# Kernel optimization log

Hardware: AMD Instinct MI355X
Metric: run time of the kernel (lower is better)

Reference implementation:

```python
import jax, jax.numpy as jnp
import numpy as np

HID = 512       # hidden_dim (embed/LSTM input)
HDE = 512       # hidden_dim_de == attn_channels (required by conv_att channel count)
NCLS = 7000
LSEQ = 40
B = 128
FH, FW = 8, 32


def setup_inputs() -> dict:
    key = jax.random.key(0)
    ks = jax.random.split(key, 16)
    s = 0.05
    inp = {
        "hidden_en": jax.random.normal(ks[0], (1, B, HID), jnp.float32),
        "x_em": jax.random.normal(ks[1], (B, HDE, FH, FW), jnp.float32),
        "att_x_em": jax.random.normal(ks[2], (B, FH * FW, HDE), jnp.float32),
        "target": jax.random.randint(ks[3], (B, LSEQ), 0, NCLS),
        "feature_h": FH,
        "feature_w": FW,
        # parameters
        "embed_w": jax.random.normal(ks[4], (NCLS, HID), jnp.float32) * s,
        "W_ih": jax.random.normal(ks[5], (4 * HDE, HID), jnp.float32) * s,   # LSTMCell input weights (i,f,g,o)
        "W_hh": jax.random.normal(ks[6], (4 * HDE, HDE), jnp.float32) * s,
        "b_ih": jax.random.normal(ks[7], (4 * HDE,), jnp.float32) * s,
        "b_hh": jax.random.normal(ks[8], (4 * HDE,), jnp.float32) * s,
        "hem_w": jax.random.normal(ks[9], (HDE, HDE), jnp.float32) * s,     # 1x1 conv h_em as matrix
        "hem_b": jax.random.normal(ks[10], (HDE,), jnp.float32) * s,
        "attw_w": jax.random.normal(ks[11], (HDE,), jnp.float32) * s,       # 1x1 conv conv_att -> 1 channel
        "attw_b": jax.random.normal(ks[12], (), jnp.float32) * s,
        "lin_w": jax.random.normal(ks[13], (NCLS, HDE + HDE), jnp.float32) * s,
        "lin_b": jax.random.normal(ks[14], (NCLS,), jnp.float32) * s,
    }
    return inp


def _decode(hidden_en, x_em, att_x_em, target, embed_w, W_ih, W_hh, b_ih, b_hh,
            hem_w, hem_b, attw_w, attw_b, lin_w, lin_b):
    L = target.shape[1]
    # teacher-forced inputs: step 0 uses hidden_en[-1], step t>=1 uses embed(target[:, t-1])
    xt0 = hidden_en[-1]                                   # [B, HID]
    xts = jnp.concatenate([xt0[None], jnp.transpose(embed_w[target[:, : L - 1]], (1, 0, 2))], axis=0)  # [L,B,HID]
    xg_all = jnp.einsum('lbi,gi->lbg', xts, W_ih) + b_ih  # precompute input gates [L,B,4H]
    Bn = x_em.shape[0]
    h0 = jnp.zeros((Bn, HDE), x_em.dtype)
    c0 = jnp.zeros((Bn, HDE), x_em.dtype)

    def step(carry, xg):
        h, c = carry
        gates = xg + h @ W_hh.T + b_hh
        i, f, g, o = jnp.split(gates, 4, axis=-1)
        c = jax.nn.sigmoid(f) * c + jax.nn.sigmoid(i) * jnp.tanh(g)
        h = jax.nn.sigmoid(o) * jnp.tanh(c)
        # additive attention (dropout treated as identity for determinism)
        hem = h @ hem_w.T + hem_b                          # [B, C]
        feat = jnp.tanh(x_em + hem[:, :, None, None])      # [B, C, H, W]
        feat_att = jnp.einsum('bchw,c->bhw', feat, attw_w) + attw_b
        alpha = jax.nn.softmax(feat_att.reshape(Bn, -1), axis=-1)  # [B, HW]
        att = jnp.einsum('bn,bnd->bd', alpha, att_x_em)    # [B, C]
        scores = jax.nn.log_softmax(jnp.concatenate([h, att], -1) @ lin_w.T + lin_b)
        return (h, c), scores

    _, ys = jax.lax.scan(step, (h0, c0), xg_all)           # ys: [L, B, NCLS]
    return jnp.transpose(ys, (1, 0, 2))                    # [B, L, NCLS]


def reference(hidden_en, x_em, att_x_em, target, feature_h, feature_w,
              embed_w, W_ih, W_hh, b_ih, b_hh, hem_w, hem_b, attw_w, attw_b,
              lin_w, lin_b):
    return _decode(hidden_en, x_em, att_x_em, target, embed_w, W_ih, W_hh,
                   b_ih, b_hh, hem_w, hem_b, attw_w, attw_b, lin_w, lin_b)
```

## Files before the change

### kernel.cpp

```cpp
#include <hip/hip_runtime.h>

#define B_    128
#define HIDD  512
#define NCLS  7000
#define NPAD  7040
#define LSEQ  40
#define MROWS 5120

typedef __attribute__((ext_vector_type(8))) short bf16x8;
typedef __attribute__((ext_vector_type(4))) float f32x4;

__device__ __forceinline__ unsigned short f2bf(float x) {
  union { float f; unsigned u; } v; v.f = x;
  unsigned r = v.u + 0x7fffu + ((v.u >> 16) & 1u);
  return (unsigned short)(r >> 16);
}
__device__ __forceinline__ float bf2f(unsigned short h) {
  union { unsigned u; float f; } v; v.u = ((unsigned)h) << 16;
  return v.f;
}
__device__ __forceinline__ float sigm(float x) { return 1.f / (1.f + __expf(-x)); }
__device__ __forceinline__ float tanh_f(float x) {
  float e = __expf(2.f * x);
  return 1.f - 2.f / (e + 1.f);
}

__global__ __launch_bounds__(256) void k_cvt(const float* __restrict__ src,
                                             unsigned short* __restrict__ dst, int n4) {
  int i = blockIdx.x * 256 + threadIdx.x;
  if (i >= n4) return;
  float4 v = ((const float4*)src)[i];
  ushort4 o; o.x = f2bf(v.x); o.y = f2bf(v.y); o.z = f2bf(v.z); o.w = f2bf(v.w);
  ((ushort4*)dst)[i] = o;
}

__global__ __launch_bounds__(256) void k_linpad(const float* __restrict__ lw,
                                                unsigned short* __restrict__ dst) {
  int i = blockIdx.x * 256 + threadIdx.x;
  int e = i * 4;
  int row = e >> 10;
  ushort4 o;
  if (row < NCLS) {
    float4 v = *(const float4*)(lw + (size_t)row * 1024 + (e & 1023));
    o.x = f2bf(v.x); o.y = f2bf(v.y); o.z = f2bf(v.z); o.w = f2bf(v.w);
  } else { o.x = 0; o.y = 0; o.z = 0; o.w = 0; }
  ((ushort4*)dst)[i] = o;
}

__global__ __launch_bounds__(256) void k_xts(const float* __restrict__ hidden_en,
                                             const float* __restrict__ embed_w,
                                             const int* __restrict__ target,
                                             unsigned short* __restrict__ xts) {
  int i = blockIdx.x * 256 + threadIdx.x;
  int e = i * 4;
  int r = e >> 9, col = e & 511;
  int l = r >> 7, b = r & 127;
  const float* src;
  if (l == 0) src = hidden_en + b * 512 + col;
  else        src = embed_w + (size_t)target[b * LSEQ + (l - 1)] * 512 + col;
  float4 v = *(const float4*)src;
  ushort4 o; o.x = f2bf(v.x); o.y = f2bf(v.y); o.z = f2bf(v.z); o.w = f2bf(v.w);
  ((ushort4*)xts)[i] = o;
}

template <int MODE>
__global__ __launch_bounds__(256) void k_gemm(const unsigned short* __restrict__ A, int lda,
                                              const unsigned short* __restrict__ Bw, int ldb,
                                              const float* __restrict__ bias,
                                              void* __restrict__ outp, int ldc, int K) {
  __shared__ __align__(16) unsigned short As[128 * 32];
  __shared__ __align__(16) unsigned short Bs[128 * 32];
  const int tid = threadIdx.x;
  const int lane = tid & 63, wid = tid >> 6;
  const int wm = wid >> 1, wn = wid & 1;
  const int quad = lane >> 4, l16 = lane & 15;
  const int m0 = blockIdx.x * 128, n0 = blockIdx.y * 128;
  f32x4 acc[4][4];
#pragma unroll
  for (int i = 0; i < 4; i++)
#pragma unroll
    for (int j = 0; j < 4; j++) acc[i][j] = (f32x4){0.f, 0.f, 0.f, 0.f};

  const int r0 = tid >> 2, kq0 = (tid & 3) * 8;
  for (int k0 = 0; k0 < K; k0 += 32) {
#pragma unroll
    for (int s = 0; s < 2; s++) {
      int row = r0 + s * 64;
      *(bf16x8*)(As + row * 32 + kq0) = *(const bf16x8*)(A + (size_t)(m0 + row) * lda + k0 + kq0);
      *(bf16x8*)(Bs + row * 32 + kq0) = *(const bf16x8*)(Bw + (size_t)(n0 + row) * ldb + k0 + kq0);
    }
    __syncthreads();
    bf16x8 af[4], bfr[4];
#pragma unroll
    for (int i = 0; i < 4; i++)
      af[i] = *(const bf16x8*)(As + (wm * 64 + i * 16 + l16) * 32 + quad * 8);
#pragma unroll
    for (int j = 0; j < 4; j++)
      bfr[j] = *(const bf16x8*)(Bs + (wn * 64 + j * 16 + l16) * 32 + quad * 8);
#pragma unroll
    for (int i = 0; i < 4; i++)
#pragma unroll
      for (int j = 0; j < 4; j++)
        acc[i][j] = __builtin_amdgcn_mfma_f32_16x16x32_bf16(af[i], bfr[j], acc[i][j], 0, 0, 0);
    __syncthreads();
  }
#pragma unroll
  for (int i = 0; i < 4; i++) {
    int mbase = m0 + wm * 64 + i * 16 + quad * 4;
#pragma unroll
    for (int j = 0; j < 4; j++) {
      int n = n0 + wn * 64 + j * 16 + l16;
#pragma unroll
      for (int r = 0; r < 4; r++) {
        float v = acc[i][j][r];
        int m = mbase + r;
        if (MODE == 0) {
          ((unsigned short*)outp)[(size_t)m * ldc + n] = f2bf(v + bias[n]);
        } else if (MODE == 1) {
          ((float*)outp)[(size_t)m * ldc + n] = v + bias[n];
        } else {
          if (n < NCLS) {
            int t = m >> 7, b = m & 127;
            ((float*)outp)[((size_t)(b * LSEQ + t)) * NCLS + n] = v + bias[n];
          }
        }
      }
    }
  }
}

__global__ __launch_bounds__(256) void k_gates(const float* __restrict__ h_prev,
                                               float* __restrict__ h_new,
                                               float* __restrict__ c_buf,
                                               const unsigned short* __restrict__ xg,
                                               const float* __restrict__ W_hh,
                                               const float* __restrict__ b_hh,
                                               unsigned short* __restrict__ hatt, int t) {
  __shared__ float h_s[16][68];
  __shared__ float W_s[64][68];
  const int tid = threadIdx.x;
  const int mt = blockIdx.x >> 5, jt = blockIdx.x & 31;
  const int m0 = mt * 16, j0 = jt * 16;
  const int mi = tid >> 4, ji = tid & 15;
  float a0 = 0.f, a1 = 0.f, a2 = 0.f, a3 = 0.f;
  if (t > 0) {
    for (int k0 = 0; k0 < 512; k0 += 64) {
      {
        int row = tid >> 4, c4 = (tid & 15) * 4;
        *(float4*)&h_s[row][c4] = *(const float4*)&h_prev[(m0 + row) * 512 + k0 + c4];
      }
#pragma unroll
      for (int w = 0; w < 4; w++) {
        int lin = w * 256 + tid;
        int row = lin >> 4, c4 = (lin & 15) * 4;
        int g = row >> 4, jj = row & 15;
        *(float4*)&W_s[row][c4] = *(const float4*)&W_hh[(size_t)((g << 9) + j0 + jj) * 512 + k0 + c4];
      }
      __syncthreads();
#pragma unroll 4
      for (int kk = 0; kk < 64; kk += 4) {
        float4 hv = *(const float4*)&h_s[mi][kk];
        float4 w0 = *(const float4*)&W_s[ji][kk];
        float4 w1 = *(const float4*)&W_s[16 + ji][kk];
        float4 w2 = *(const float4*)&W_s[32 + ji][kk];
        float4 w3 = *(const float4*)&W_s[48 + ji][kk];
        a0 += hv.x * w0.x + hv.y * w0.y + hv.z * w0.z + hv.w * w0.w;
        a1 += hv.x * w1.x + hv.y * w1.y + hv.z * w1.z + hv.w * w1.w;
        a2 += hv.x * w2.x + hv.y * w2.y + hv.z * w2.z + hv.w * w2.w;
        a3 += hv.x * w3.x + hv.y * w3.y + hv.z * w3.z + hv.w * w3.w;
      }
      __syncthreads();
    }
  }
  const int m = m0 + mi, j = j0 + ji;
  const size_t r = (size_t)t * 128 + m;
  a0 += bf2f(xg[r * 2048 + j])          + b_hh[j];
  a1 += bf2f(xg[r * 2048 + 512 + j])    + b_hh[512 + j];
  a2 += bf2f(xg[r * 2048 + 1024 + j])   + b_hh[1024 + j];
  a3 += bf2f(xg[r * 2048 + 1536 + j])   + b_hh[1536 + j];
  float ig = sigm(a0), fg = sigm(a1), gg = tanh_f(a2), og = sigm(a3);
  float c_old = (t > 0) ? c_buf[m * 512 + j] : 0.f;
  float c = fg * c_old + ig * gg;
  float h = og * tanh_f(c);
  c_buf[m * 512 + j] = c;
  h_new[m * 512 + j] = h;
  hatt[r * 1024 + j] = f2bf(h);
}

__global__ __launch_bounds__(256) void k_feat(const float* __restrict__ hem_all,
                                              const unsigned short* __restrict__ xem,
                                              const float* __restrict__ attw_w,
                                              float* __restrict__ s_all) {
  __shared__ float hemL[512], wL[512], sp[2][128];
  const int tid = threadIdx.x;
  const int t = blockIdx.x >> 8;
  const int rem = blockIdx.x & 255;
  const int b = rem >> 1, ph = rem & 1;
  const size_t hrow = ((size_t)t * 128 + b) * 512;
  hemL[tid] = hem_all[hrow + tid];
  hemL[256 + tid] = hem_all[hrow + 256 + tid];
  wL[tid] = attw_w[tid];
  wL[256 + tid] = attw_w[256 + tid];
  __syncthreads();
  const int pl = tid & 127, ch = tid >> 7;
  const int p = ph * 128 + pl;
  const unsigned short* xp = xem + ((size_t)b * 512 + ch * 256) * 256 + p;
  float acc = 0.f;
#pragma unroll 4
  for (int ci = 0; ci < 256; ci++) {
    int c = ch * 256 + ci;
    float x = bf2f(xp[(size_t)ci * 256]);
    acc += wL[c] * tanh_f(x + hemL[c]);
  }
  sp[ch][pl] = acc;
  __syncthreads();
  if (ch == 0)
    s_all[((size_t)t * 128 + b) * 256 + p] = sp[0][pl] + sp[1][pl];
}

__global__ __launch_bounds__(256) void k_att(const float* __restrict__ s_all,
                                             const float* __restrict__ atx,
                                             unsigned short* __restrict__ hatt) {
  __shared__ float sL[40][257];
  __shared__ float zinv[40];
  const int tid = threadIdx.x;
  const int b = blockIdx.x >> 1, dh = blockIdx.x & 1;
  for (int i = tid; i < 40 * 256; i += 256) {
    int t = i >> 8, p = i & 255;
    sL[t][p] = s_all[((size_t)t * 128 + b) * 256 + p];
  }
  __syncthreads();
  if (tid < 40) {
    int t = tid;
    float mx = -1e30f;
    for (int p = 0; p < 256; p++) mx = fmaxf(mx, sL[t][p]);
    float z = 0.f;
    for (int p = 0; p < 256; p++) { float e = __expf(sL[t][p] - mx); sL[t][p] = e; z += e; }
    zinv[t] = 1.f / z;
  }
  __syncthreads();
  float acc[40];
#pragma unroll
  for (int t = 0; t < 40; t++) acc[t] = 0.f;
  const int d = dh * 256 + tid;
  const float* ap = atx + (size_t)b * 256 * 512 + d;
  for (int p = 0; p < 256; p++) {
    float av = ap[(size_t)p * 512];
#pragma unroll
    for (int t = 0; t < 40; t++) acc[t] += sL[t][p] * av;
  }
#pragma unroll
  for (int t = 0; t < 40; t++) {
    float v = acc[t] * zinv[t];
    hatt[((size_t)t * 128 + b) * 1024 + 512 + d] = f2bf(v);
  }
}

__global__ __launch_bounds__(256) void k_lsm(float* __restrict__ out) {
  __shared__ float buf[7000];
  __shared__ float red[256];
  const int tid = threadIdx.x;
  float* pr = out + (size_t)blockIdx.x * NCLS;
  for (int i = tid * 4; i < NCLS; i += 1024)
    *(float4*)&buf[i] = *(const float4*)&pr[i];
  __syncthreads();
  float mx = -1e30f;
  for (int i = tid; i < NCLS; i += 256) mx = fmaxf(mx, buf[i]);
  red[tid] = mx; __syncthreads();
  for (int s = 128; s > 0; s >>= 1) { if (tid < s) red[tid] = fmaxf(red[tid], red[tid + s]); __syncthreads(); }
  mx = red[0]; __syncthreads();
  float sum = 0.f;
  for (int i = tid; i < NCLS; i += 256) sum += __expf(buf[i] - mx);
  red[tid] = sum; __syncthreads();
  for (int s = 128; s > 0; s >>= 1) { if (tid < s) red[tid] += red[tid + s]; __syncthreads(); }
  float lse = mx + __logf(red[0]);
  for (int i = tid * 4; i < NCLS; i += 1024) {
    float4 v = *(const float4*)&buf[i];
    v.x -= lse; v.y -= lse; v.z -= lse; v.w -= lse;
    *(float4*)&pr[i] = v;
  }
}

extern "C" void kernel_launch(void* const* d_in, const int* in_sizes, int n_in,
                              void* d_out, int out_size, void* d_ws, size_t ws_size,
                              hipStream_t stream) {
  const float* hidden_en = (const float*)d_in[0];
  const float* x_em      = (const float*)d_in[1];
  const float* att_x     = (const float*)d_in[2];
  const int*   target    = (const int*)d_in[3];
  const float* embed_w   = (const float*)d_in[6];
  const float* W_ih      = (const float*)d_in[7];
  const float* W_hh      = (const float*)d_in[8];
  const float* b_ih      = (const float*)d_in[9];
  const float* b_hh      = (const float*)d_in[10];
  const float* hem_w     = (const float*)d_in[11];
  const float* hem_b     = (const float*)d_in[12];
  const float* attw_w    = (const float*)d_in[13];
  const float* lin_w     = (const float*)d_in[15];
  const float* lin_b     = (const float*)d_in[16];
  float* out = (float*)d_out;
  (void)in_sizes; (void)n_in; (void)out_size; (void)ws_size;

  char* w = (char*)d_ws;
  size_t off = 0;
  auto alloc = [&](size_t bytes) { char* p = w + off; off = (off + bytes + 255) & ~(size_t)255; return p; };
  unsigned short* xts  = (unsigned short*)alloc((size_t)MROWS * 512 * 2);
  unsigned short* wih  = (unsigned short*)alloc((size_t)2048 * 512 * 2);
  unsigned short* xg   = (unsigned short*)alloc((size_t)MROWS * 2048 * 2);
  unsigned short* hemw = (unsigned short*)alloc((size_t)512 * 512 * 2);
  unsigned short* linw = (unsigned short*)alloc((size_t)NPAD * 1024 * 2);
  unsigned short* xem  = (unsigned short*)alloc((size_t)128 * 512 * 256 * 2);
  unsigned short* hatt = (unsigned short*)alloc((size_t)MROWS * 1024 * 2);
  float* h0      = (float*)alloc((size_t)128 * 512 * 4);
  float* h1      = (float*)alloc((size_t)128 * 512 * 4);
  float* cb      = (float*)alloc((size_t)128 * 512 * 4);
  float* hem_all = (float*)alloc((size_t)MROWS * 512 * 4);
  float* s_all   = (float*)alloc((size_t)MROWS * 256 * 4);

  k_cvt<<<1024, 256, 0, stream>>>(W_ih, wih, 2048 * 512 / 4);
  k_cvt<<<256, 256, 0, stream>>>(hem_w, hemw, 512 * 512 / 4);
  k_cvt<<<16384, 256, 0, stream>>>(x_em, xem, 128 * 512 * 256 / 4);
  k_linpad<<<NPAD * 1024 / 4 / 256, 256, 0, stream>>>(lin_w, linw);
  k_xts<<<MROWS * 512 / 4 / 256, 256, 0, stream>>>(hidden_en, embed_w, target, xts);
  k_gemm<0><<<dim3(40, 16), 256, 0, stream>>>(xts, 512, wih, 512, b_ih, xg, 2048, 512);

  for (int t = 0; t < LSEQ; t++) {
    const float* hp = (t & 1) ? h0 : h1;
    float* hn = (t & 1) ? h1 : h0;
    k_gates<<<256, 256, 0, stream>>>(hp, hn, cb, xg, W_hh, b_hh, hatt, t);
  }

  k_gemm<1><<<dim3(40, 4), 256, 0, stream>>>(hatt, 1024, hemw, 512, hem_b, hem_all, 512, 512);
  k_feat<<<LSEQ * 256, 256, 0, stream>>>(hem_all, xem, attw_w, s_all);
  k_att<<<256, 256, 0, stream>>>(s_all, att_x, hatt);

  k_gemm<2><<<dim3(40, 55), 256, 0, stream>>>(hatt, 1024, linw, 1024, lin_b, out, NCLS, 1024);
  k_lsm<<<MROWS, 256, 0, stream>>>(out);
}
```

Baseline: 1.642 ms.

## Factor tanh into exp products and reuse x_em across timesteps in attention

Rewrites tanh(x+h) as 1 - 2/(e^{2x}·e^{2h}+1). x_em is pre-exponentiated once at conversion, and the hem GEMM epilogue now emits exp(2·hem). This leaves the attention inner loop with one FMA plus one hardware reciprocal per element, since the constant term cancels in the softmax. The attention kernel is also restructured so each block handles 10 timesteps for one batch row, loading each x_em element once and reusing it across those steps. The risks are overflow or inf in exp for large inputs, bf16 precision loss on stored exponentials, and fewer blocks (512) with higher register use.

```diff
diff --git a/kernel.cpp b/kernel.cpp
--- a/kernel.cpp
+++ b/kernel.cpp
@@ -6,6 +6,7 @@
 #define NPAD  7040
 #define LSEQ  40
 #define MROWS 5120
+#define TT    10
 
 typedef __attribute__((ext_vector_type(8))) short bf16x8;
 typedef __attribute__((ext_vector_type(4))) float f32x4;
@@ -24,6 +25,7 @@
   float e = __expf(2.f * x);
   return 1.f - 2.f / (e + 1.f);
 }
+__device__ __forceinline__ float rcp_f(float x) { return __builtin_amdgcn_rcpf(x); }
 
 __global__ __launch_bounds__(256) void k_cvt(const float* __restrict__ src,
                                              unsigned short* __restrict__ dst, int n4) {
@@ -31,6 +33,17 @@
   if (i >= n4) return;
   float4 v = ((const float4*)src)[i];
   ushort4 o; o.x = f2bf(v.x); o.y = f2bf(v.y); o.z = f2bf(v.z); o.w = f2bf(v.w);
+  ((ushort4*)dst)[i] = o;
+}
+
+__global__ __launch_bounds__(256) void k_expcvt(const float* __restrict__ src,
+                                                unsigned short* __restrict__ dst, int n4) {
+  int i = blockIdx.x * 256 + threadIdx.x;
+  if (i >= n4) return;
+  float4 v = ((const float4*)src)[i];
+  ushort4 o;
+  o.x = f2bf(__expf(2.f * v.x)); o.y = f2bf(__expf(2.f * v.y));
+  o.z = f2bf(__expf(2.f * v.z)); o.w = f2bf(__expf(2.f * v.w));
   ((ushort4*)dst)[i] = o;
 }
 
@@ -116,8 +129,8 @@
         int m = mbase + r;
         if (MODE == 0) {
           ((unsigned short*)outp)[(size_t)m * ldc + n] = f2bf(v + bias[n]);
-        } else if (MODE == 1) {
-          ((float*)outp)[(size_t)m * ldc + n] = v + bias[n];
+        } else if (MODE == 3) {
+          ((float*)outp)[(size_t)m * ldc + n] = __expf(2.f * (v + bias[n]));
         } else {
           if (n < NCLS) {
             int t = m >> 7, b = m & 127;
@@ -187,35 +200,44 @@
   hatt[r * 1024 + j] = f2bf(h);
 }
 
-__global__ __launch_bounds__(256) void k_feat(const float* __restrict__ hem_all,
-                                              const unsigned short* __restrict__ xem,
+__global__ __launch_bounds__(256) void k_feat(const float* __restrict__ Eh,
+                                              const unsigned short* __restrict__ Ex,
                                               const float* __restrict__ attw_w,
                                               float* __restrict__ s_all) {
-  __shared__ float hemL[512], wL[512], sp[2][128];
-  const int tid = threadIdx.x;
-  const int t = blockIdx.x >> 8;
-  const int rem = blockIdx.x & 255;
-  const int b = rem >> 1, ph = rem & 1;
-  const size_t hrow = ((size_t)t * 128 + b) * 512;
-  hemL[tid] = hem_all[hrow + tid];
-  hemL[256 + tid] = hem_all[hrow + 256 + tid];
-  wL[tid] = attw_w[tid];
-  wL[256 + tid] = attw_w[256 + tid];
+  __shared__ float EhL[TT][512];
+  __shared__ float wL[512];
+  const int tid = threadIdx.x;
+  const int tg = blockIdx.x >> 7, b = blockIdx.x & 127;
+  const int t0 = tg * TT;
+  for (int i = tid * 4; i < TT * 512; i += 1024) {
+    int t = i >> 9, c = i & 511;
+    *(float4*)&EhL[t][c] = *(const float4*)&Eh[((size_t)(t0 + t) * 128 + b) * 512 + c];
+  }
+  if (tid < 128) *(float4*)&wL[tid * 4] = *(const float4*)&attw_w[tid * 4];
   __syncthreads();
-  const int pl = tid & 127, ch = tid >> 7;
-  const int p = ph * 128 + pl;
-  const unsigned short* xp = xem + ((size_t)b * 512 + ch * 256) * 256 + p;
-  float acc = 0.f;
-#pragma unroll 4
-  for (int ci = 0; ci < 256; ci++) {
-    int c = ch * 256 + ci;
-    float x = bf2f(xp[(size_t)ci * 256]);
-    acc += wL[c] * tanh_f(x + hemL[c]);
-  }
-  sp[ch][pl] = acc;
-  __syncthreads();
-  if (ch == 0)
-    s_all[((size_t)t * 128 + b) * 256 + p] = sp[0][pl] + sp[1][pl];
+  const int p = tid;
+  const unsigned short* xp = Ex + (size_t)b * 512 * 256 + p;
+  float acc[TT];
+#pragma unroll
+  for (int t = 0; t < TT; t++) acc[t] = 0.f;
+  for (int c0 = 0; c0 < 512; c0 += 4) {
+    float ex0 = bf2f(xp[(size_t)(c0 + 0) * 256]);
+    float ex1 = bf2f(xp[(size_t)(c0 + 1) * 256]);
+    float ex2 = bf2f(xp[(size_t)(c0 + 2) * 256]);
+    float ex3 = bf2f(xp[(size_t)(c0 + 3) * 256]);
+    float4 wv = *(const float4*)&wL[c0];
+#pragma unroll
+    for (int t = 0; t < TT; t++) {
+      float4 eh = *(const float4*)&EhL[t][c0];
+      acc[t] = __builtin_fmaf(wv.x, rcp_f(__builtin_fmaf(ex0, eh.x, 1.f)), acc[t]);
+      acc[t] = __builtin_fmaf(wv.y, rcp_f(__builtin_fmaf(ex1, eh.y, 1.f)), acc[t]);
+      acc[t] = __builtin_fmaf(wv.z, rcp_f(__builtin_fmaf(ex2, eh.z, 1.f)), acc[t]);
+      acc[t] = __builtin_fmaf(wv.w, rcp_f(__builtin_fmaf(ex3, eh.w, 1.f)), acc[t]);
+    }
+  }
+#pragma unroll
+  for (int t = 0; t < TT; t++)
+    s_all[((size_t)(t0 + t) * 128 + b) * 256 + p] = -2.f * acc[t];
 }
 
 __global__ __launch_bounds__(256) void k_att(const float* __restrict__ s_all,
@@ -314,12 +336,12 @@
   float* h0      = (float*)alloc((size_t)128 * 512 * 4);
   float* h1      = (float*)alloc((size_t)128 * 512 * 4);
   float* cb      = (float*)alloc((size_t)128 * 512 * 4);
-  float* hem_all = (float*)alloc((size_t)MROWS * 512 * 4);
+  float* eh_all  = (float*)alloc((size_t)MROWS * 512 * 4);
   float* s_all   = (float*)alloc((size_t)MROWS * 256 * 4);
 
   k_cvt<<<1024, 256, 0, stream>>>(W_ih, wih, 2048 * 512 / 4);
   k_cvt<<<256, 256, 0, stream>>>(hem_w, hemw, 512 * 512 / 4);
-  k_cvt<<<16384, 256, 0, stream>>>(x_em, xem, 128 * 512 * 256 / 4);
+  k_expcvt<<<16384, 256, 0, stream>>>(x_em, xem, 128 * 512 * 256 / 4);
   k_linpad<<<NPAD * 1024 / 4 / 256, 256, 0, stream>>>(lin_w, linw);
   k_xts<<<MROWS * 512 / 4 / 256, 256, 0, stream>>>(hidden_en, embed_w, target, xts);
   k_gemm<0><<<dim3(40, 16), 256, 0, stream>>>(xts, 512, wih, 512, b_ih, xg, 2048, 512);
@@ -330,8 +352,8 @@
     k_gates<<<256, 256, 0, stream>>>(hp, hn, cb, xg, W_hh, b_hh, hatt, t);
   }
 
-  k_gemm<1><<<dim3(40, 4), 256, 0, stream>>>(hatt, 1024, hemw, 512, hem_b, hem_all, 512, 512);
-  k_feat<<<LSEQ * 256, 256, 0, stream>>>(hem_all, xem, attw_w, s_all);
+  k_gemm<3><<<dim3(40, 4), 256, 0, stream>>>(hatt, 1024, hemw, 512, hem_b, eh_all, 512, 512);
+  k_feat<<<512, 256, 0, stream>>>(eh_all, xem, attw_w, s_all);
   k_att<<<256, 256, 0, stream>>>(s_all, att_x, hatt);
 
   k_gemm<2><<<dim3(40, 55), 256, 0, stream>>>(hatt, 1024, linw, 1024, lin_b, out, NCLS, 1024);
```

Measured after the change: 1.395 ms. 15.0% less time.
